# Kernel tuning notes

Measured on AMD Instinct MI355X. Metric: run time of the kernel, lower is better.

Reference implementation:

```python
import jax, jax.numpy as jnp
import numpy as np

EPS = 1e-15
MAX_NORM = 1.0 - 1e-5

def _norm(x):
    return jnp.sqrt(jnp.maximum(jnp.sum(x * x, -1, keepdims=True), EPS))

def project(x):
    n = _norm(x)
    return jnp.where(n > MAX_NORM, x * (MAX_NORM / n), x)

def mobius_add(x, y):
    x2 = jnp.sum(x * x, -1, keepdims=True)
    y2 = jnp.sum(y * y, -1, keepdims=True)
    xy = jnp.sum(x * y, -1, keepdims=True)
    num = (1.0 + 2.0 * xy + y2) * x + (1.0 - x2) * y
    den = 1.0 + 2.0 * xy + x2 * y2
    return num / jnp.maximum(den, EPS)

def expmap0(u):
    n = _norm(u)
    return jnp.tanh(n) * u / n

def expmap(u, p):
    lam = 2.0 / jnp.maximum(1.0 - jnp.sum(p * p, -1, keepdims=True), EPS)
    n = _norm(u)
    return mobius_add(p, jnp.tanh(0.5 * lam * n) * u / n)

def logmap(x, p):
    sub = mobius_add(-p, x)
    n = _norm(sub)
    lam = 2.0 / jnp.maximum(1.0 - jnp.sum(p * p, -1, keepdims=True), EPS)
    return (2.0 / lam) * jnp.arctanh(jnp.minimum(n, MAX_NORM)) * sub / n

def seg_mean(msg, idx, n):
    s = jax.ops.segment_sum(msg, idx, num_segments=n)
    c = jax.ops.segment_sum(jnp.ones((idx.shape[0], 1), msg.dtype), idx, num_segments=n)
    return s / jnp.maximum(c, 1.0)  # zero in-degree -> 0, matching DGL mean


def setup_inputs() -> dict:
    N_ENT, N_USR, N_ITM, N_REL, D = 100000, 50000, 30000, 40, 64
    E_KG, E_CF = 800000, 600000
    key = jax.random.key(0)
    ks = jax.random.split(key, 12)
    return {
        "entity_embed": 0.1 * jax.random.normal(ks[0], (N_ENT, D), jnp.float32),
        "user_embed": 0.1 * jax.random.normal(ks[1], (N_USR, D), jnp.float32),
        "relation_emb": 0.1 * jax.random.normal(ks[2], (N_REL, D), jnp.float32),
        "W1": jax.random.normal(ks[3], (D, D), jnp.float32) / np.sqrt(D),
        "W2": jax.random.normal(ks[4], (D, D), jnp.float32) / np.sqrt(D),
        "kg_src": jax.random.randint(ks[5], (E_KG,), 0, N_ENT, jnp.int32),
        "kg_dst": jax.random.randint(ks[6], (E_KG,), 0, N_ENT, jnp.int32),
        "kg_type": jax.random.randint(ks[7], (E_KG,), 0, N_REL - 2, jnp.int32),
        "iu_src": jax.random.randint(ks[8], (E_CF,), 0, N_ITM, jnp.int32),
        "iu_dst": N_ITM + jax.random.randint(ks[9], (E_CF,), 0, N_USR, jnp.int32),
        "ui_src": N_ITM + jax.random.randint(ks[10], (E_CF,), 0, N_USR, jnp.int32),
        "ui_dst": jax.random.randint(ks[11], (E_CF,), 0, N_ITM, jnp.int32),
        "n_items": N_ITM,
    }


def reference(entity_embed, user_embed, relation_emb, W1, W2,
              kg_src, kg_dst, kg_type, iu_src, iu_dst, ui_src, ui_dst, n_items):
    n_ent = entity_embed.shape[0]
    n_usr = user_embed.shape[0]
    N = n_items + n_usr

    # --- per-edge hyperbolic UDF (tan_sum) on the KG graph ---
    p = expmap0(entity_embed[kg_src])                 # [E, d] tangent origin at src
    dst_h = expmap(entity_embed[kg_dst], p)
    rel_h = expmap(relation_emb[kg_type + 2], p)
    tan_sum = logmap(project(mobius_add(dst_h, rel_h)), p)
    # sg_inv reverses edges, so mean groups by the ORIGINAL src node
    out = seg_mean(tan_sum, kg_src, n_ent)            # [n_ent, d]

    # --- CF scatter-means over item/user bipartite graphs ---
    cat_nodes = jnp.concatenate([out[:n_items], user_embed], axis=0)  # [N, d]
    u = seg_mean(cat_nodes[iu_src], iu_dst, N)[n_items:]              # [n_usr, d]

    norm_all = jnp.sum(cat_nodes * cat_nodes, -1, keepdims=True)      # ||.||^2, [N,1]
    node_n = cat_nodes / (norm_all + 1e-6)
    msg = node_n[ui_src] * norm_all[ui_dst]                           # u_mul_v
    i_cf = seg_mean(msg, ui_dst, N)[:n_items]                         # [n_items, d]

    # --- gated fusion ---
    out_items = out[:n_items]
    gi = jax.nn.sigmoid(out_items @ W1.T + i_cf @ W2.T)
    item_emb_fusion = gi * out_items + (1.0 - gi) * i_cf

    return (jnp.concatenate([item_emb_fusion, out[n_items:]], axis=0), u, out_items)
```

## Files before the change

### kernel.cpp

```cpp
#include <hip/hip_runtime.h>
#include <cstdint>

#define EPSF 1e-15f
#define MAXN (1.0f - 1e-5f)
#define BSH 9

typedef __attribute__((ext_vector_type(8))) short bf16x8;
typedef __attribute__((ext_vector_type(4))) float f32x4;

__device__ __forceinline__ float wsum64(float v) {
    v += __shfl_xor(v, 1);
    v += __shfl_xor(v, 2);
    v += __shfl_xor(v, 4);
    v += __shfl_xor(v, 8);
    v += __shfl_xor(v, 16);
    v += __shfl_xor(v, 32);
    return v;
}

__device__ __forceinline__ float dot4(float4 a, float4 b) {
    return a.x * b.x + a.y * b.y + a.z * b.z + a.w * b.w;
}

__device__ __forceinline__ float frcp(float x) {
    return __builtin_amdgcn_rcpf(x);
}

__device__ __forceinline__ float tanh_f(float x) {
    x = fminf(x, 10.f);
    float t = __expf(2.f * x);
    return (t - 1.f) * frcp(t + 1.f);
}

__device__ __forceinline__ float atanh_f(float x) {
    return 0.5f * __logf((1.f + x) * frcp(1.f - x));
}

__device__ __forceinline__ short f2bf(float f) {
    uint32_t b = __float_as_uint(f);
    b = (b + 0x7FFF + ((b >> 16) & 1)) >> 16;
    return (short)b;
}

__device__ __forceinline__ bf16x8 pack8(const float* __restrict__ p) {
    float4 lo = *(const float4*)p;
    float4 hi = *(const float4*)(p + 4);
    bf16x8 r;
    r[0] = f2bf(lo.x); r[1] = f2bf(lo.y); r[2] = f2bf(lo.z); r[3] = f2bf(lo.w);
    r[4] = f2bf(hi.x); r[5] = f2bf(hi.y); r[6] = f2bf(hi.z); r[7] = f2bf(hi.w);
    return r;
}


__global__ __launch_bounds__(256) void p1_hist_k(
        const int* __restrict__ kg_src, const int* __restrict__ iu_dst,
        const int* __restrict__ ui_dst, int* __restrict__ H,
        int E_kg, int E_iu, int E_ui, int n_items, int S1, int SU, int nbins) {
    __shared__ int h[512];
    int tid = threadIdx.x;
    h[tid] = 0; h[tid + 256] = 0;
    __syncthreads();
    long tot = (long)E_kg + E_iu + E_ui;
    long b0 = (long)blockIdx.x * 2048 + tid;
#pragma unroll
    for (int j = 0; j < 8; ++j) {
        long t = b0 + (long)j * 256;
        if (t < tot) {
            int slot;
            if (t < E_kg) slot = kg_src[t];
            else if (t < (long)E_kg + E_iu) slot = S1 + iu_dst[t - E_kg] - n_items;
            else slot = S1 + SU + ui_dst[t - E_kg - E_iu];
            atomicAdd(&h[slot >> BSH], 1);
        }
    }
    __syncthreads();
    int* row = H + (size_t)blockIdx.x * nbins;
    if (tid < nbins) row[tid] = h[tid];
    if (tid + 256 < nbins) row[tid + 256] = h[tid + 256];
}

__global__ __launch_bounds__(256) void p2a_scan_k(int* __restrict__ H,
        int* __restrict__ binTotal, int NBLK, int nbins) {
    int bin = blockIdx.x, tid = threadIdx.x;
    int lane = tid & 63, w = tid >> 6;
    __shared__ int wtot[4];
    int carry = 0;
    for (int c0 = 0; c0 < NBLK; c0 += 256) {
        int idx = c0 + tid;
        int v = (idx < NBLK) ? H[(size_t)idx * nbins + bin] : 0;
        int inc = v;
#pragma unroll
        for (int off = 1; off < 64; off <<= 1) {
            int u = __shfl_up(inc, off);
            if (lane >= off) inc += u;
        }
        if (lane == 63) wtot[w] = inc;
        __syncthreads();
        int woff = 0;
        for (int i = 0; i < w; ++i) woff += wtot[i];
        int ctot = wtot[0] + wtot[1] + wtot[2] + wtot[3];
        if (idx < NBLK) H[(size_t)idx * nbins + bin] = carry + woff + inc - v;
        carry += ctot;
        __syncthreads();
    }
    if (tid == 0) binTotal[bin] = carry;
}

__global__ __launch_bounds__(512) void p2b_bins_k(const int* __restrict__ binTotal,
        int* __restrict__ binStart, int nbins) {
    int tid = threadIdx.x, lane = tid & 63, w = tid >> 6;
    __shared__ int wtot[8];
    int v = (tid < nbins) ? binTotal[tid] : 0;
    int inc = v;
#pragma unroll
    for (int off = 1; off < 64; off <<= 1) {
        int u = __shfl_up(inc, off);
        if (lane >= off) inc += u;
    }
    if (lane == 63) wtot[w] = inc;
    __syncthreads();
    int woff = 0;
    for (int i = 0; i < w; ++i) woff += wtot[i];
    if (tid < nbins) binStart[tid] = woff + inc - v;
    if (tid == 0) {
        int tot = 0;
        for (int i = 0; i < 8; ++i) tot += wtot[i];
        binStart[nbins] = tot;
    }
}

__global__ __launch_bounds__(256) void p3_scat_k(
        const int* __restrict__ kg_src, const int* __restrict__ kg_dst,
        const int* __restrict__ kg_typ, const int* __restrict__ iu_src,
        const int* __restrict__ iu_dst, const int* __restrict__ ui_src,
        const int* __restrict__ ui_dst,
        const int* __restrict__ H, const int* __restrict__ binStart,
        int2* __restrict__ recA,
        int E_kg, int E_iu, int E_ui, int n_items, int S1, int SU, int nbins) {
    __shared__ int off[512];
    int tid = threadIdx.x;
    const int* row = H + (size_t)blockIdx.x * nbins;
    if (tid < nbins) off[tid] = binStart[tid] + row[tid];
    if (tid + 256 < nbins) off[tid + 256] = binStart[tid + 256] + row[tid + 256];
    __syncthreads();
    long tot = (long)E_kg + E_iu + E_ui;
    long b0 = (long)blockIdx.x * 2048 + tid;
#pragma unroll
    for (int j = 0; j < 8; ++j) {
        long t = b0 + (long)j * 256;
        if (t < tot) {
            int slot, aux;
            if (t < E_kg) {
                slot = kg_src[t];
                aux = kg_dst[t] | ((kg_typ[t] + 2) << 18);
            } else if (t < (long)E_kg + E_iu) {
                long e = t - E_kg;
                slot = S1 + iu_dst[e] - n_items;
                aux = iu_src[e];
            } else {
                long e = t - E_kg - E_iu;
                slot = S1 + SU + ui_dst[e];
                aux = ui_src[e];
            }
            int pos = atomicAdd(&off[slot >> BSH], 1);
            recA[pos] = make_int2(slot, aux);
        }
    }
}

__global__ __launch_bounds__(256) void p4_sort_k(
        const int2* __restrict__ recA, const int* __restrict__ binStart,
        int2* __restrict__ recB, int* __restrict__ deg, int* __restrict__ base,
        int nbins) {
    int b = blockIdx.x, tid = threadIdx.x;
    int lane = tid & 63, w = tid >> 6;
    int lo = binStart[b], cnt = binStart[b + 1] - lo;
    __shared__ int h[512];
    __shared__ int pre[512];
    __shared__ int wtot[4];
    h[tid] = 0; h[tid + 256] = 0;
    __syncthreads();
    for (int i = tid; i < cnt; i += 256)
        atomicAdd(&h[recA[lo + i].x & 511], 1);
    __syncthreads();
    int v1 = h[tid];
    int inc = v1;
#pragma unroll
    for (int off = 1; off < 64; off <<= 1) {
        int u = __shfl_up(inc, off);
        if (lane >= off) inc += u;
    }
    if (lane == 63) wtot[w] = inc;
    __syncthreads();
    int woff = 0;
    for (int i = 0; i < w; ++i) woff += wtot[i];
    int T1 = wtot[0] + wtot[1] + wtot[2] + wtot[3];
    int p1 = woff + inc - v1;
    __syncthreads();
    int v2 = h[tid + 256];
    inc = v2;
#pragma unroll
    for (int off = 1; off < 64; off <<= 1) {
        int u = __shfl_up(inc, off);
        if (lane >= off) inc += u;
    }
    if (lane == 63) wtot[w] = inc;
    __syncthreads();
    woff = 0;
    for (int i = 0; i < w; ++i) woff += wtot[i];
    int p2 = T1 + woff + inc - v2;
    pre[tid] = p1; pre[tid + 256] = p2;
    int slot0 = (b << BSH) + tid;
    deg[slot0] = v1;       base[slot0] = lo + p1;
    deg[slot0 + 256] = v2; base[slot0 + 256] = lo + p2;
    __syncthreads();
    for (int i = tid; i < cnt; i += 256) {
        int2 r = recA[lo + i];
        int p = atomicAdd(&pre[r.x & 511], 1);
        recB[lo + p] = r;
    }
}


__global__ __launch_bounds__(256) void kg_edge_fused_k(const float* __restrict__ ent,
                          const float* __restrict__ rel,
                          const int2* __restrict__ rec,
                          float4* __restrict__ payload,
                          int nE) {
    int w = blockIdx.x * 4 + (threadIdx.x >> 6);
    int l = threadIdx.x & 63;
    int slot = w * 16 + (l >> 2);
    if (slot >= nE) return;
    int j0 = l & 3;
    int2 rc = rec[slot];
    int s = rc.x, d = rc.y & 0x3FFFF, ty = rc.y >> 18;
    const float4* pu = (const float4*)(ent + (size_t)s * 64);
    const float4* pv = (const float4*)(ent + (size_t)d * 64);
    const float4* pr = (const float4*)(rel + (size_t)ty * 64);

    float uu = 0.f, vv = 0.f, rr = 0.f, uv = 0.f, ur = 0.f, vr = 0.f;
#pragma unroll
    for (int i = 0; i < 4; ++i) {
        float4 a = pu[4 * i + j0], b = pv[4 * i + j0], c = pr[4 * i + j0];
        uu += dot4(a, a); vv += dot4(b, b); rr += dot4(c, c);
        uv += dot4(a, b); ur += dot4(a, c); vr += dot4(b, c);
    }
#pragma unroll
    for (int m = 1; m < 4; m <<= 1) {
        uu += __shfl_xor(uu, m);
        vv += __shfl_xor(vv, m);
        rr += __shfl_xor(rr, m);
        uv += __shfl_xor(uv, m);
        ur += __shfl_xor(ur, m);
        vr += __shfl_xor(vr, m);
    }

    float n0 = sqrtf(fmaxf(uu, EPSF));
    float cp = tanh_f(n0) * frcp(n0);
    float p2 = cp * cp * uu;
    float om_p2 = 1.f - p2;
    float lam = 2.f * frcp(fmaxf(om_p2, EPSF));

    float nv = sqrtf(fmaxf(vv, EPSF));
    float cd = tanh_f(0.5f * lam * nv) * frcp(nv);
    float wd2 = cd * cd * vv;
    float pwd = cp * cd * uv;
    float iDd = frcp(fmaxf(1.f + 2.f * pwd + p2 * wd2, EPSF));
    float a1 = (1.f + 2.f * pwd + wd2) * cp * iDd;
    float b1 = om_p2 * cd * iDd;

    float nr = sqrtf(fmaxf(rr, EPSF));
    float cr = tanh_f(0.5f * lam * nr) * frcp(nr);
    float wr2 = cr * cr * rr;
    float pwr = cp * cr * ur;
    float iDr = frcp(fmaxf(1.f + 2.f * pwr + p2 * wr2, EPSF));
    float a2 = (1.f + 2.f * pwr + wr2) * cp * iDr;
    float c2 = om_p2 * cr * iDr;

    float x2 = a1 * a1 * uu + 2.f * a1 * b1 * uv + b1 * b1 * vv;
    float y2 = a2 * a2 * uu + 2.f * a2 * c2 * ur + c2 * c2 * rr;
    float xy = a1 * a2 * uu + a1 * c2 * ur + b1 * a2 * uv + b1 * c2 * vr;
    float iden = frcp(fmaxf(1.f + 2.f * xy + x2 * y2, EPSF));
    float E = (1.f + 2.f * xy + y2) * iden;
    float F = (1.f - x2) * iden;
    float zu = E * a1 + F * a2;
    float zv = E * b1;
    float zr = F * c2;

    float z2 = zu * zu * uu + zv * zv * vv + zr * zr * rr
             + 2.f * (zu * zv * uv + zu * zr * ur + zv * zr * vr);
    float nz = sqrtf(fmaxf(z2, EPSF));
    if (nz > MAXN) {
        float sc = MAXN * frcp(nz);
        zu *= sc; zv *= sc; zr *= sc;
        z2 *= sc * sc;
    }

    float mxy = -cp * (zu * uu + zv * uv + zr * ur);
    float idenl = frcp(fmaxf(1.f + 2.f * mxy + p2 * z2, EPSF));
    float G = (1.f + 2.f * mxy + z2) * idenl;
    float H = om_p2 * idenl;
    float su = -G * cp + H * zu;
    float sv = H * zv;
    float sr = H * zr;

    float ns2 = su * su * uu + sv * sv * vv + sr * sr * rr
              + 2.f * (su * sv * uv + su * sr * ur + sv * sr * vr);
    float ns = sqrtf(fmaxf(ns2, EPSF));
    float k = fmaxf(om_p2, EPSF) * atanh_f(fminf(ns, MAXN)) * frcp(ns);

    if (j0 == 0) {
        payload[slot] = make_float4(k * sv, k * sr, k * su, __int_as_float(rc.y));
    }
}

__global__ void kg_gather_k(const float* __restrict__ ent,
                            const float* __restrict__ rel,
                            const int* __restrict__ deg,
                            const int* __restrict__ base,
                            const float4* __restrict__ payload,
                            float* __restrict__ out_final,
                            float* __restrict__ out_items,
                            float* __restrict__ normv,
                            int n_items, int n) {
    int w = blockIdx.x * (blockDim.x >> 6) + (threadIdx.x >> 6);
    int i0 = w * 2;
    if (i0 >= n) return;
    bool has1 = (i0 + 1 < n);
    int l = threadIdx.x & 63;
    int b0 = base[i0];
    int d0 = deg[i0];
    int d1 = has1 ? deg[i0 + 1] : 0;
    int cnt = d0 + d1;
    int split = b0 + d0;
    float acc0 = 0.f, as0 = 0.f, acc1 = 0.f, as1 = 0.f;
    int q = 0;
    for (; q + 8 <= cnt; q += 8) {
        float4 p[8]; float vv[8], rr_[8];
#pragma unroll
        for (int j = 0; j < 8; ++j) p[j] = payload[b0 + q + j];
#pragma unroll
        for (int j = 0; j < 8; ++j) {
            int wd = __float_as_int(p[j].w);
            vv[j] = ent[(size_t)(wd & 0x3FFFF) * 64 + l];
            rr_[j] = rel[(size_t)(wd >> 18) * 64 + l];
        }
#pragma unroll
        for (int j = 0; j < 8; ++j) {
            float t = p[j].x * vv[j] + p[j].y * rr_[j];
            bool s0 = (b0 + q + j) < split;
            acc0 += s0 ? t : 0.f;
            acc1 += s0 ? 0.f : t;
            as0 += s0 ? p[j].z : 0.f;
            as1 += s0 ? 0.f : p[j].z;
        }
    }
    for (; q < cnt; ++q) {
        float4 p = payload[b0 + q];
        int wd = __float_as_int(p.w);
        float t = p.x * ent[(size_t)(wd & 0x3FFFF) * 64 + l]
                + p.y * rel[(size_t)(wd >> 18) * 64 + l];
        bool s0 = (b0 + q) < split;
        acc0 += s0 ? t : 0.f;
        acc1 += s0 ? 0.f : t;
        as0 += s0 ? p.z : 0.f;
        as1 += s0 ? 0.f : p.z;
    }
    {
        float v = (acc0 + as0 * ent[(size_t)i0 * 64 + l]) * frcp(fmaxf((float)d0, 1.f));
        if (i0 < n_items) {
            out_items[(size_t)i0 * 64 + l] = v;
            float s2 = wsum64(v * v);
            if (l == 0) normv[i0] = s2;
        } else {
            out_final[(size_t)i0 * 64 + l] = v;
        }
    }
    if (has1) {
        int i1 = i0 + 1;
        float v = (acc1 + as1 * ent[(size_t)i1 * 64 + l]) * frcp(fmaxf((float)d1, 1.f));
        if (i1 < n_items) {
            out_items[(size_t)i1 * 64 + l] = v;
            float s2 = wsum64(v * v);
            if (l == 0) normv[i1] = s2;
        } else {
            out_final[(size_t)i1 * 64 + l] = v;
        }
    }
}

__global__ void user_norm_k(const float* __restrict__ user, float* __restrict__ normv,
                            int n_items, int n_usr) {
    int j = blockIdx.x * (blockDim.x >> 6) + (threadIdx.x >> 6);
    if (j >= n_usr) return;
    int l = threadIdx.x & 63;
    float c = user[(size_t)j * 64 + l];
    float s = wsum64(c * c);
    if (l == 0) normv[n_items + j] = s;
}


__global__ void iu_gather_k(const float* __restrict__ items, const float* __restrict__ user,
                            const int* __restrict__ deg, const int* __restrict__ base,
                            const int2* __restrict__ rec,
                            float* __restrict__ out_u, int n_items, int n, int SOFF) {
    int w = blockIdx.x * (blockDim.x >> 6) + (threadIdx.x >> 6);
    int i0 = w * 2;
    if (i0 >= n) return;
    bool has1 = (i0 + 1 < n);
    int l = threadIdx.x & 63;
    int b0 = base[SOFF + i0];
    int d0 = deg[SOFF + i0];
    int d1 = has1 ? deg[SOFF + i0 + 1] : 0;
    int cnt = d0 + d1;
    int split = b0 + d0;
    float acc0 = 0.f, acc1 = 0.f;
    int q = 0;
    for (; q + 8 <= cnt; q += 8) {
        float vs[8]; bool s0[8];
#pragma unroll
        for (int j = 0; j < 8; ++j) {
            int sidx = rec[b0 + q + j].y;
            vs[j] = (sidx < n_items) ? items[(size_t)sidx * 64 + l]
                                     : user[(size_t)(sidx - n_items) * 64 + l];
            s0[j] = (b0 + q + j) < split;
        }
#pragma unroll
        for (int j = 0; j < 8; ++j) {
            acc0 += s0[j] ? vs[j] : 0.f;
            acc1 += s0[j] ? 0.f : vs[j];
        }
    }
    for (; q < cnt; ++q) {
        int sidx = rec[b0 + q].y;
        float v = (sidx < n_items) ? items[(size_t)sidx * 64 + l]
                                   : user[(size_t)(sidx - n_items) * 64 + l];
        bool s0 = (b0 + q) < split;
        acc0 += s0 ? v : 0.f;
        acc1 += s0 ? 0.f : v;
    }
    out_u[(size_t)i0 * 64 + l] = acc0 * frcp(fmaxf((float)d0, 1.f));
    if (has1)
        out_u[(size_t)(i0 + 1) * 64 + l] = acc1 * frcp(fmaxf((float)d1, 1.f));
}

__global__ void ui_gather_k(const float* __restrict__ items, const float* __restrict__ user,
                            const float* __restrict__ normv,
                            const int* __restrict__ deg, const int* __restrict__ base,
                            const int2* __restrict__ rec,
                            float* __restrict__ icf, int n_items, int n, int SOFF) {
    int w = blockIdx.x * (blockDim.x >> 6) + (threadIdx.x >> 6);
    int i0 = w * 2;
    if (i0 >= n) return;
    bool has1 = (i0 + 1 < n);
    int l = threadIdx.x & 63;
    int b0 = base[SOFF + i0];
    int d0 = deg[SOFF + i0];
    int d1 = has1 ? deg[SOFF + i0 + 1] : 0;
    int cnt = d0 + d1;
    int split = b0 + d0;
    float acc0 = 0.f, acc1 = 0.f;
    int q = 0;
    for (; q + 8 <= cnt; q += 8) {
        int ss[8]; float fs[8], vs[8]; bool s0[8];
#pragma unroll
        for (int j = 0; j < 8; ++j) ss[j] = rec[b0 + q + j].y;
#pragma unroll
        for (int j = 0; j < 8; ++j) fs[j] = frcp(normv[ss[j]] + 1e-6f);
#pragma unroll
        for (int j = 0; j < 8; ++j) {
            int sidx = ss[j];
            vs[j] = (sidx < n_items) ? items[(size_t)sidx * 64 + l]
                                     : user[(size_t)(sidx - n_items) * 64 + l];
            s0[j] = (b0 + q + j) < split;
        }
#pragma unroll
        for (int j = 0; j < 8; ++j) {
            float t = fs[j] * vs[j];
            acc0 += s0[j] ? t : 0.f;
            acc1 += s0[j] ? 0.f : t;
        }
    }
    for (; q < cnt; ++q) {
        int sidx = rec[b0 + q].y;
        float f = frcp(normv[sidx] + 1e-6f);
        float t = f * ((sidx < n_items) ? items[(size_t)sidx * 64 + l]
                                        : user[(size_t)(sidx - n_items) * 64 + l]);
        bool s0 = (b0 + q) < split;
        acc0 += s0 ? t : 0.f;
        acc1 += s0 ? 0.f : t;
    }
    icf[(size_t)i0 * 64 + l] = normv[i0] * acc0 * frcp(fmaxf((float)d0, 1.f));
    if (has1)
        icf[(size_t)(i0 + 1) * 64 + l] =
            normv[i0 + 1] * acc1 * frcp(fmaxf((float)d1, 1.f));
}

__global__ __launch_bounds__(256) void fusion_mfma_k(const float* __restrict__ items,
                          const float* __restrict__ icf,
                          const float* __restrict__ W1, const float* __restrict__ W2,
                          float* __restrict__ outf, int n_items) {
    int lane = threadIdx.x & 63;
    int row0 = blockIdx.x * 64 + (threadIdx.x >> 6) * 16;
    int r = lane & 15, g = lane >> 4;

    int arow = row0 + r;
    size_t rbase = (size_t)(arow < n_items ? arow : 0) * 64;

    bf16x8 afrag[4];
#pragma unroll
    for (int s = 0; s < 4; ++s) {
        int kb = s * 32 + g * 8;
        const float* p = (kb < 64) ? (items + rbase + kb) : (icf + rbase + kb - 64);
        afrag[s] = pack8(p);
    }

    bf16x8 bfrag[4][4];
#pragma unroll
    for (int c = 0; c < 4; ++c) {
        int col = c * 16 + r;
#pragma unroll
        for (int s = 0; s < 4; ++s) {
            int kb = s * 32 + g * 8;
            const float* p = (kb < 64) ? (W1 + col * 64 + kb) : (W2 + col * 64 + kb - 64);
            bfrag[c][s] = pack8(p);
        }
    }

    f32x4 acc[4] = {{0.f,0.f,0.f,0.f},{0.f,0.f,0.f,0.f},
                    {0.f,0.f,0.f,0.f},{0.f,0.f,0.f,0.f}};
#pragma unroll
    for (int s = 0; s < 4; ++s)
#pragma unroll
        for (int c = 0; c < 4; ++c)
            acc[c] = __builtin_amdgcn_mfma_f32_16x16x32_bf16(afrag[s], bfrag[c][s],
                                                             acc[c], 0, 0, 0);

#pragma unroll
    for (int c = 0; c < 4; ++c) {
        int col = c * 16 + r;
#pragma unroll
        for (int q = 0; q < 4; ++q) {
            int orow = row0 + g * 4 + q;
            if (orow < n_items) {
                size_t off = (size_t)orow * 64 + col;
                float oi = items[off], cf = icf[off];
                float gate = frcp(1.f + __expf(-acc[c][q]));
                outf[off] = gate * oi + (1.f - gate) * cf;
            }
        }
    }
}

extern "C" void kernel_launch(void* const* d_in, const int* in_sizes, int n_in,
                              void* d_out, int out_size, void* d_ws, size_t ws_size,
                              hipStream_t stream) {
    const float* ent    = (const float*)d_in[0];
    const float* usr    = (const float*)d_in[1];
    const float* rel    = (const float*)d_in[2];
    const float* W1     = (const float*)d_in[3];
    const float* W2     = (const float*)d_in[4];
    const int*   kg_src = (const int*)d_in[5];
    const int*   kg_dst = (const int*)d_in[6];
    const int*   kg_typ = (const int*)d_in[7];
    const int*   iu_src = (const int*)d_in[8];
    const int*   iu_dst = (const int*)d_in[9];
    const int*   ui_src = (const int*)d_in[10];
    const int*   ui_dst = (const int*)d_in[11];

    const int n_ent   = in_sizes[0] / 64;
    const int n_usr   = in_sizes[1] / 64;
    const int E_kg    = in_sizes[5];
    const int E_iu    = in_sizes[8];
    const int E_ui    = in_sizes[10];
    const int n_items = (out_size - in_sizes[0] - in_sizes[1]) / 64;
    const int N       = n_items + n_usr;

    const int S1 = ((n_ent + 511) / 512) * 512;
    const int SU = ((n_usr + 511) / 512) * 512;
    const int SI = ((n_items + 511) / 512) * 512;
    const int S3 = S1 + SU + SI;
    const int nbins = S3 >> BSH;
    const long tot = (long)E_kg + E_iu + E_ui;
    const int NBLK = (int)((tot + 2047) / 2048);

    float* out_final = (float*)d_out;
    float* out_u     = out_final + (size_t)n_ent * 64;
    float* out_items = out_u + (size_t)n_usr * 64;

    int2* recA = (int2*)out_u;
    int*  H    = (int*)(recA + tot);

    float* ws = (float*)d_ws;
    size_t o = 0;
    int* binTotal = (int*)(ws + o); o += nbins;
    int* binStart = (int*)(ws + o); o += nbins + 1;
    int* deg      = (int*)(ws + o); o += S3;
    int* basep    = (int*)(ws + o); o += S3;
    o = (o + 3) & ~(size_t)3;
    int2* recB    = (int2*)(ws + o); o += (size_t)tot * 2;
    float4* pay_kg = (float4*)(ws + o); o += (size_t)E_kg * 4;
    float* icf    = (float*)pay_kg;
    float* normv  = ws + o; o += N;

    p1_hist_k<<<NBLK, 256, 0, stream>>>(kg_src, iu_dst, ui_dst, H,
                                        E_kg, E_iu, E_ui, n_items, S1, SU, nbins);
    p2a_scan_k<<<nbins, 256, 0, stream>>>(H, binTotal, NBLK, nbins);
    p2b_bins_k<<<1, 512, 0, stream>>>(binTotal, binStart, nbins);
    p3_scat_k<<<NBLK, 256, 0, stream>>>(kg_src, kg_dst, kg_typ, iu_src, iu_dst,
                                        ui_src, ui_dst, H, binStart, recA,
                                        E_kg, E_iu, E_ui, n_items, S1, SU, nbins);
    p4_sort_k<<<nbins, 256, 0, stream>>>(recA, binStart, recB, deg, basep, nbins);

    kg_edge_fused_k<<<(E_kg + 63) / 64, 256, 0, stream>>>(ent, rel, recB,
                                                          pay_kg, E_kg);
    int wv_e = (n_ent + 1) / 2;
    kg_gather_k<<<(wv_e + 3) / 4, 256, 0, stream>>>(ent, rel, deg, basep, pay_kg,
                                                    out_final, out_items, normv,
                                                    n_items, n_ent);
    user_norm_k<<<(n_usr + 3) / 4, 256, 0, stream>>>(usr, normv, n_items, n_usr);

    int wv_u = (n_usr + 1) / 2;
    iu_gather_k<<<(wv_u + 3) / 4, 256, 0, stream>>>(out_items, usr, deg, basep,
                                                    recB, out_u, n_items, n_usr, S1);
    int wv_i = (n_items + 1) / 2;
    ui_gather_k<<<(wv_i + 3) / 4, 256, 0, stream>>>(out_items, usr, normv, deg,
                                                    basep, recB, icf, n_items,
                                                    n_items, S1 + SU);
    fusion_mfma_k<<<(n_items + 63) / 64, 256, 0, stream>>>(out_items, icf, W1, W2,
                                                           out_final, n_items);
}
```

Baseline: 234.5 us.

## Gather neighbor embeddings from bf16 shadow copies in KG and CF kernels

Adds a conversion kernel that writes bf16 copies of the entity, user and relation tables. kg_gather now writes a bf16 concatenated item/user table alongside its fp32 output. The KG and CF gather kernels read these half-width rows instead of fp32, which halves the bytes fetched per random gather and removes the item/user branch. In exchange it adds an extra conversion pass over the full tables plus extra stores, and aggregates bf16-rounded values, which may loosen accuracy.

```diff
diff --git a/kernel.cpp b/kernel.cpp
--- a/kernel.cpp
+++ b/kernel.cpp
@@ -7,6 +7,7 @@
 
 typedef __attribute__((ext_vector_type(8))) short bf16x8;
 typedef __attribute__((ext_vector_type(4))) float f32x4;
+typedef unsigned short ushort_t;
 
 __device__ __forceinline__ float wsum64(float v) {
     v += __shfl_xor(v, 1);
@@ -36,19 +37,44 @@
     return 0.5f * __logf((1.f + x) * frcp(1.f - x));
 }
 
-__device__ __forceinline__ short f2bf(float f) {
+__device__ __forceinline__ ushort_t f2bf(float f) {
     uint32_t b = __float_as_uint(f);
     b = (b + 0x7FFF + ((b >> 16) & 1)) >> 16;
-    return (short)b;
+    return (ushort_t)b;
+}
+
+__device__ __forceinline__ float bf2f(ushort_t h) {
+    return __uint_as_float((uint32_t)h << 16);
 }
 
 __device__ __forceinline__ bf16x8 pack8(const float* __restrict__ p) {
     float4 lo = *(const float4*)p;
     float4 hi = *(const float4*)(p + 4);
     bf16x8 r;
-    r[0] = f2bf(lo.x); r[1] = f2bf(lo.y); r[2] = f2bf(lo.z); r[3] = f2bf(lo.w);
-    r[4] = f2bf(hi.x); r[5] = f2bf(hi.y); r[6] = f2bf(hi.z); r[7] = f2bf(hi.w);
+    r[0] = (short)f2bf(lo.x); r[1] = (short)f2bf(lo.y);
+    r[2] = (short)f2bf(lo.z); r[3] = (short)f2bf(lo.w);
+    r[4] = (short)f2bf(hi.x); r[5] = (short)f2bf(hi.y);
+    r[6] = (short)f2bf(hi.z); r[7] = (short)f2bf(hi.w);
     return r;
+}
+
+__global__ __launch_bounds__(256) void cvt3_k(
+        const float* __restrict__ ent, const float* __restrict__ usr,
+        const float* __restrict__ rel,
+        ushort_t* __restrict__ entH, ushort_t* __restrict__ usrH,
+        ushort_t* __restrict__ relH, long nE, long nU, long nR) {
+    long i = ((long)blockIdx.x * blockDim.x + threadIdx.x) * 8;
+    const float* s; ushort_t* d; long off;
+    if (i < nE) { s = ent; d = entH; off = i; }
+    else if (i < nE + nU) { s = usr; d = usrH; off = i - nE; }
+    else if (i < nE + nU + nR) { s = rel; d = relH; off = i - nE - nU; }
+    else return;
+    float4 a = *(const float4*)(s + off);
+    float4 b = *(const float4*)(s + off + 4);
+    ushort4 lo; lo.x = f2bf(a.x); lo.y = f2bf(a.y); lo.z = f2bf(a.z); lo.w = f2bf(a.w);
+    ushort4 hi; hi.x = f2bf(b.x); hi.y = f2bf(b.y); hi.z = f2bf(b.z); hi.w = f2bf(b.w);
+    *(ushort4*)(d + off) = lo;
+    *(ushort4*)(d + off + 4) = hi;
 }
 
 
@@ -315,12 +341,14 @@
 }
 
 __global__ void kg_gather_k(const float* __restrict__ ent,
-                            const float* __restrict__ rel,
+                            const ushort_t* __restrict__ entH,
+                            const ushort_t* __restrict__ relH,
                             const int* __restrict__ deg,
                             const int* __restrict__ base,
                             const float4* __restrict__ payload,
                             float* __restrict__ out_final,
                             float* __restrict__ out_items,
+                            ushort_t* __restrict__ catH,
                             float* __restrict__ normv,
                             int n_items, int n) {
     int w = blockIdx.x * (blockDim.x >> 6) + (threadIdx.x >> 6);
@@ -342,8 +370,8 @@
 #pragma unroll
         for (int j = 0; j < 8; ++j) {
             int wd = __float_as_int(p[j].w);
-            vv[j] = ent[(size_t)(wd & 0x3FFFF) * 64 + l];
-            rr_[j] = rel[(size_t)(wd >> 18) * 64 + l];
+            vv[j] = bf2f(entH[(size_t)(wd & 0x3FFFF) * 64 + l]);
+            rr_[j] = bf2f(relH[(size_t)(wd >> 18) * 64 + l]);
         }
 #pragma unroll
         for (int j = 0; j < 8; ++j) {
@@ -358,8 +386,8 @@
     for (; q < cnt; ++q) {
         float4 p = payload[b0 + q];
         int wd = __float_as_int(p.w);
-        float t = p.x * ent[(size_t)(wd & 0x3FFFF) * 64 + l]
-                + p.y * rel[(size_t)(wd >> 18) * 64 + l];
+        float t = p.x * bf2f(entH[(size_t)(wd & 0x3FFFF) * 64 + l])
+                + p.y * bf2f(relH[(size_t)(wd >> 18) * 64 + l]);
         bool s0 = (b0 + q) < split;
         acc0 += s0 ? t : 0.f;
         acc1 += s0 ? 0.f : t;
@@ -370,6 +398,7 @@
         float v = (acc0 + as0 * ent[(size_t)i0 * 64 + l]) * frcp(fmaxf((float)d0, 1.f));
         if (i0 < n_items) {
             out_items[(size_t)i0 * 64 + l] = v;
+            catH[(size_t)i0 * 64 + l] = f2bf(v);
             float s2 = wsum64(v * v);
             if (l == 0) normv[i0] = s2;
         } else {
@@ -381,6 +410,7 @@
         float v = (acc1 + as1 * ent[(size_t)i1 * 64 + l]) * frcp(fmaxf((float)d1, 1.f));
         if (i1 < n_items) {
             out_items[(size_t)i1 * 64 + l] = v;
+            catH[(size_t)i1 * 64 + l] = f2bf(v);
             float s2 = wsum64(v * v);
             if (l == 0) normv[i1] = s2;
         } else {
@@ -400,10 +430,10 @@
 }
 
 
-__global__ void iu_gather_k(const float* __restrict__ items, const float* __restrict__ user,
+__global__ void iu_gather_k(const ushort_t* __restrict__ catH,
                             const int* __restrict__ deg, const int* __restrict__ base,
                             const int2* __restrict__ rec,
-                            float* __restrict__ out_u, int n_items, int n, int SOFF) {
+                            float* __restrict__ out_u, int n, int SOFF) {
     int w = blockIdx.x * (blockDim.x >> 6) + (threadIdx.x >> 6);
     int i0 = w * 2;
     if (i0 >= n) return;
@@ -421,8 +451,7 @@
 #pragma unroll
         for (int j = 0; j < 8; ++j) {
             int sidx = rec[b0 + q + j].y;
-            vs[j] = (sidx < n_items) ? items[(size_t)sidx * 64 + l]
-                                     : user[(size_t)(sidx - n_items) * 64 + l];
+            vs[j] = bf2f(catH[(size_t)sidx * 64 + l]);
             s0[j] = (b0 + q + j) < split;
         }
 #pragma unroll
@@ -433,8 +462,7 @@
     }
     for (; q < cnt; ++q) {
         int sidx = rec[b0 + q].y;
-        float v = (sidx < n_items) ? items[(size_t)sidx * 64 + l]
-                                   : user[(size_t)(sidx - n_items) * 64 + l];
+        float v = bf2f(catH[(size_t)sidx * 64 + l]);
         bool s0 = (b0 + q) < split;
         acc0 += s0 ? v : 0.f;
         acc1 += s0 ? 0.f : v;
@@ -444,11 +472,11 @@
         out_u[(size_t)(i0 + 1) * 64 + l] = acc1 * frcp(fmaxf((float)d1, 1.f));
 }
 
-__global__ void ui_gather_k(const float* __restrict__ items, const float* __restrict__ user,
+__global__ void ui_gather_k(const ushort_t* __restrict__ catH,
                             const float* __restrict__ normv,
                             const int* __restrict__ deg, const int* __restrict__ base,
                             const int2* __restrict__ rec,
-                            float* __restrict__ icf, int n_items, int n, int SOFF) {
+                            float* __restrict__ icf, int n, int SOFF) {
     int w = blockIdx.x * (blockDim.x >> 6) + (threadIdx.x >> 6);
     int i0 = w * 2;
     if (i0 >= n) return;
@@ -469,9 +497,7 @@
         for (int j = 0; j < 8; ++j) fs[j] = frcp(normv[ss[j]] + 1e-6f);
 #pragma unroll
         for (int j = 0; j < 8; ++j) {
-            int sidx = ss[j];
-            vs[j] = (sidx < n_items) ? items[(size_t)sidx * 64 + l]
-                                     : user[(size_t)(sidx - n_items) * 64 + l];
+            vs[j] = bf2f(catH[(size_t)ss[j] * 64 + l]);
             s0[j] = (b0 + q + j) < split;
         }
 #pragma unroll
@@ -483,9 +509,7 @@
     }
     for (; q < cnt; ++q) {
         int sidx = rec[b0 + q].y;
-        float f = frcp(normv[sidx] + 1e-6f);
-        float t = f * ((sidx < n_items) ? items[(size_t)sidx * 64 + l]
-                                        : user[(size_t)(sidx - n_items) * 64 + l]);
+        float t = frcp(normv[sidx] + 1e-6f) * bf2f(catH[(size_t)sidx * 64 + l]);
         bool s0 = (b0 + q) < split;
         acc0 += s0 ? t : 0.f;
         acc1 += s0 ? 0.f : t;
@@ -570,6 +594,7 @@
 
     const int n_ent   = in_sizes[0] / 64;
     const int n_usr   = in_sizes[1] / 64;
+    const int n_rel   = in_sizes[2] / 64;
     const int E_kg    = in_sizes[5];
     const int E_iu    = in_sizes[8];
     const int E_ui    = in_sizes[10];
@@ -602,6 +627,17 @@
     float4* pay_kg = (float4*)(ws + o); o += (size_t)E_kg * 4;
     float* icf    = (float*)pay_kg;
     float* normv  = ws + o; o += N;
+    o = (o + 3) & ~(size_t)3;
+    ushort_t* entH = (ushort_t*)(ws + o); o += (size_t)n_ent * 32;
+    ushort_t* catH = (ushort_t*)(ws + o); o += (size_t)N * 32;
+    ushort_t* relH = (ushort_t*)(ws + o); o += (size_t)n_rel * 32;
+    ushort_t* usrH = catH + (size_t)n_items * 64;
+
+    long nE64 = (long)n_ent * 64, nU64 = (long)n_usr * 64, nR64 = (long)n_rel * 64;
+    long tcvt = (nE64 + nU64 + nR64) / 8;
+    cvt3_k<<<(int)((tcvt + 255) / 256), 256, 0, stream>>>(ent, usr, rel,
+                                                          entH, usrH, relH,
+                                                          nE64, nU64, nR64);
 
     p1_hist_k<<<NBLK, 256, 0, stream>>>(kg_src, iu_dst, ui_dst, H,
                                         E_kg, E_iu, E_ui, n_items, S1, SU, nbins);
@@ -615,18 +651,17 @@
     kg_edge_fused_k<<<(E_kg + 63) / 64, 256, 0, stream>>>(ent, rel, recB,
                                                           pay_kg, E_kg);
     int wv_e = (n_ent + 1) / 2;
-    kg_gather_k<<<(wv_e + 3) / 4, 256, 0, stream>>>(ent, rel, deg, basep, pay_kg,
-                                                    out_final, out_items, normv,
-                                                    n_items, n_ent);
+    kg_gather_k<<<(wv_e + 3) / 4, 256, 0, stream>>>(ent, entH, relH, deg, basep,
+                                                    pay_kg, out_final, out_items,
+                                                    catH, normv, n_items, n_ent);
     user_norm_k<<<(n_usr + 3) / 4, 256, 0, stream>>>(usr, normv, n_items, n_usr);
 
     int wv_u = (n_usr + 1) / 2;
-    iu_gather_k<<<(wv_u + 3) / 4, 256, 0, stream>>>(out_items, usr, deg, basep,
-                                                    recB, out_u, n_items, n_usr, S1);
+    iu_gather_k<<<(wv_u + 3) / 4, 256, 0, stream>>>(catH, deg, basep, recB,
+                                                    out_u, n_usr, S1);
     int wv_i = (n_items + 1) / 2;
-    ui_gather_k<<<(wv_i + 3) / 4, 256, 0, stream>>>(out_items, usr, normv, deg,
-                                                    basep, recB, icf, n_items,
-                                                    n_items, S1 + SU);
+    ui_gather_k<<<(wv_i + 3) / 4, 256, 0, stream>>>(catH, normv, deg, basep, recB,
+                                                    icf, n_items, S1 + SU);
     fusion_mfma_k<<<(n_items + 63) / 64, 256, 0, stream>>>(out_items, icf, W1, W2,
                                                            out_final, n_items);
 }
```

Result: no change. 238.0 us (+1.5%).
